# Kernel optimization log

Hardware: AMD Instinct MI355X
Metric: run time of the kernel (lower is better)

The kernel has to match this reference:

```python
import jax, jax.numpy as jnp
import numpy as np

B, T, D = 16384, 3, 512   # batch, task_num, input_dim
G = T + 1                  # expert groups (idx 0 shared)
NE = 4                     # experts per group
H, E = 512, 256            # expert hidden, expert output dim (layers=[512,256])
GH = 256                   # gate hidden
TH, TO = 128, 64           # tower hidden / output dims


def setup_inputs() -> dict:
    key = jax.random.key(0)
    ks = jax.random.split(key, 14)
    s = 0.02
    return {
        "inputs": jax.random.normal(ks[0], (B, G, D), jnp.float32),
        # expert MLPs: [group, expert, ...]
        "expert_W1": jax.random.normal(ks[1], (G, NE, D, H), jnp.float32) * s,
        "expert_b1": jnp.zeros((G, NE, H), jnp.float32),
        "expert_W2": jax.random.normal(ks[2], (G, NE, H, E), jnp.float32) * s,
        "expert_b2": jnp.zeros((G, NE, E), jnp.float32),
        # per-task gates (softmax over G*NE experts)
        "gate_W1": jax.random.normal(ks[3], (T, D, GH), jnp.float32) * s,
        "gate_b1": jnp.zeros((T, GH), jnp.float32),
        "gate_W2": jax.random.normal(ks[4], (T, GH, G * NE), jnp.float32) * s,
        "gate_b2": jnp.zeros((T, G * NE), jnp.float32),
        # per-task towers (is_last=True)
        "tower_W1": jax.random.normal(ks[5], (T, E, TH), jnp.float32) * s,
        "tower_b1": jnp.zeros((T, TH), jnp.float32),
        "tower_W2": jax.random.normal(ks[6], (T, TH, TO), jnp.float32) * s,
        "tower_b2": jnp.zeros((T, TO), jnp.float32),
    }


def reference(inputs, expert_W1, expert_b1, expert_W2, expert_b2,
              gate_W1, gate_b1, gate_W2, gate_b2,
              tower_W1, tower_b1, tower_W2, tower_b2):
    b = inputs.shape[0]
    g, ne = expert_W1.shape[0], expert_W1.shape[1]
    t_num = gate_W1.shape[0]

    # All expert groups in one batched einsum: [B, G, NE, E]
    h1 = jax.nn.relu(jnp.einsum('bgd,gndh->bgnh', inputs, expert_W1) + expert_b1)
    emb = jnp.einsum('bgnh,gnhe->bgne', h1, expert_W2) + expert_b2

    # Task gates on (task input + shared input): softmax over G*NE experts
    gin = inputs[:, 1:, :] + inputs[:, :1, :]                      # [B, T, D]
    gh = jax.nn.relu(jnp.einsum('btd,tdh->bth', gin, gate_W1) + gate_b1)
    gw = jax.nn.softmax(jnp.einsum('bth,thk->btk', gh, gate_W2) + gate_b2, axis=-1)  # [B,T,G*NE]

    emb_sg = jax.lax.stop_gradient(emb)
    group_ids = jnp.arange(g)
    outs = []
    for t in range(t_num):
        # gradient flows only through shared group (0) and own group (t+1)
        keep = (group_ids == 0) | (group_ids == t + 1)              # [G]
        masked = jnp.where(keep[None, :, None, None], emb, emb_sg)  # [B,G,NE,E]
        agg = jnp.einsum('bk,bke->be', gw[:, t], masked.reshape(b, g * ne, -1))  # [B,E]
        th = jax.nn.relu(agg @ tower_W1[t] + tower_b1[t])
        outs.append(th @ tower_W2[t] + tower_b2[t])                 # [B,TO]
    return jnp.concatenate(outs, axis=1)                           # [B, T*TO]
```

## Files before the change

### kernel.cpp

```cpp
#include <hip/hip_runtime.h>
#include <math.h>

#define B_N  16384
#define T_N  3
#define D_N  512
#define G_N  4
#define NE_N 4
#define H_N  512
#define E_N  256
#define GH_N 256
#define K16  16
#define TH_N 128
#define TO_N 64

typedef __attribute__((ext_vector_type(8))) short short8;
typedef __attribute__((ext_vector_type(4))) float floatx4;

__device__ __forceinline__ unsigned short f2bf(float f) {
    union { float f; unsigned u; } v; v.f = f;
    unsigned r = (v.u + 0x7fffu + ((v.u >> 16) & 1u)) >> 16;
    return (unsigned short)r;
}
__device__ __forceinline__ float bf2f(unsigned short h) {
    union { unsigned u; float f; } v; v.u = ((unsigned)h) << 16;
    return v.f;
}
__device__ __forceinline__ unsigned pack2(float lo, float hi) {
    return ((unsigned)f2bf(hi) << 16) | (unsigned)f2bf(lo);
}

typedef const __attribute__((address_space(1))) void gvoid_t;
typedef __attribute__((address_space(3))) void lvoid_t;

#if __has_builtin(__builtin_amdgcn_global_load_lds)
#define HAVE_GLL 1
__device__ __forceinline__ void load_lds16(const void* g, void* l) {
    __builtin_amdgcn_global_load_lds((gvoid_t*)g, (lvoid_t*)l, 16, 0, 0);
}
#else
#define HAVE_GLL 0
#endif

__global__ __launch_bounds__(256) void convert_inputs(
    const float* __restrict__ x, unsigned short* __restrict__ xb,
    unsigned short* __restrict__ ginb)
{
    const long b = blockIdx.x;
    const int tid = threadIdx.x;
    const float* xr = x + b * (G_N * D_N);
    unsigned short* xo = xb + b * (G_N * D_N);
    unsigned short* go = ginb + b * (T_N * D_N);
    float2 v0 = *(const float2*)&xr[tid * 2];
    *(unsigned*)&xo[tid * 2] = pack2(v0.x, v0.y);
    #pragma unroll
    for (int g = 1; g < G_N; ++g) {
        float2 v = *(const float2*)&xr[g * D_N + tid * 2];
        *(unsigned*)&xo[g * D_N + tid * 2] = pack2(v.x, v.y);
        *(unsigned*)&go[(g - 1) * D_N + tid * 2] = pack2(v.x + v0.x, v.y + v0.y);
    }
}

__global__ __launch_bounds__(256) void transpose_w(
    const float* __restrict__ in, unsigned short* __restrict__ out, int K, int N)
{
    __shared__ float tile[32][33];
    const int tx = threadIdx.x, ty = threadIdx.y;
    const long zo = (long)blockIdx.z * K * N;
    const int n0 = blockIdx.x * 32, k0 = blockIdx.y * 32;
    #pragma unroll
    for (int i = 0; i < 4; ++i)
        tile[ty + 8 * i][tx] = in[zo + (long)(k0 + ty + 8 * i) * N + n0 + tx];
    __syncthreads();
    #pragma unroll
    for (int i = 0; i < 4; ++i)
        out[zo + (long)(n0 + ty + 8 * i) * K + k0 + tx] = f2bf(tile[tx][ty + 8 * i]);
}

template<int RELU>
__global__ __launch_bounds__(256) void gemm_bf16(
    const unsigned short* __restrict__ A, int lda, int a_zoff,
    const unsigned short* __restrict__ Bt, int bt_zoff,
    const float* __restrict__ bias, int bias_zoff,
    unsigned short* __restrict__ C, int ldc, int c_zoff, int K)
{
    __shared__ __align__(16) unsigned short As[2][128 * 32];
    __shared__ __align__(16) unsigned short Bs[2][128 * 32];
    const int tid = threadIdx.x;
    const int z = blockIdx.z;
    const long m0 = (long)blockIdx.x * 128;
    const long n0 = (long)blockIdx.y * 128;
    const unsigned short* Ab = A + (long)z * a_zoff + m0 * lda;
    const unsigned short* Bb = Bt + (long)z * bt_zoff + n0 * K;
    const int lane16 = tid & 15;
    const int quad = (tid & 63) >> 4;
    const int wave = tid >> 6;
    const int wm = (wave >> 1) * 64;
    const int wn = (wave & 1) * 64;
    const int srow = tid >> 2;
    const int scolsw = (((tid & 3) ^ ((tid >> 3) & 3)) * 8);
    const int cw8 = ((quad ^ ((lane16 >> 1) & 3)) * 8);

    floatx4 acc[4][4] = {};

    for (int k0 = 0; k0 < K; k0 += 64) {
        #pragma unroll
        for (int h = 0; h < 2; ++h) {
            const int kh = k0 + h * 32;
#if HAVE_GLL
            load_lds16(Ab + (long)srow * lda + kh + scolsw, &As[h][tid * 8]);
            load_lds16(Ab + (long)(srow + 64) * lda + kh + scolsw, &As[h][2048 + tid * 8]);
            load_lds16(Bb + (long)srow * K + kh + scolsw, &Bs[h][tid * 8]);
            load_lds16(Bb + (long)(srow + 64) * K + kh + scolsw, &Bs[h][2048 + tid * 8]);
#else
            *(uint4*)&As[h][tid * 8] = *(const uint4*)(Ab + (long)srow * lda + kh + scolsw);
            *(uint4*)&As[h][2048 + tid * 8] = *(const uint4*)(Ab + (long)(srow + 64) * lda + kh + scolsw);
            *(uint4*)&Bs[h][tid * 8] = *(const uint4*)(Bb + (long)srow * K + kh + scolsw);
            *(uint4*)&Bs[h][2048 + tid * 8] = *(const uint4*)(Bb + (long)(srow + 64) * K + kh + scolsw);
#endif
        }
        __syncthreads();
        #pragma unroll
        for (int h = 0; h < 2; ++h) {
            short8 a[4], b[4];
            #pragma unroll
            for (int mi = 0; mi < 4; ++mi)
                a[mi] = *(const short8*)&As[h][(wm + mi * 16 + lane16) * 32 + cw8];
            #pragma unroll
            for (int ni = 0; ni < 4; ++ni)
                b[ni] = *(const short8*)&Bs[h][(wn + ni * 16 + lane16) * 32 + cw8];
            #pragma unroll
            for (int mi = 0; mi < 4; ++mi)
                #pragma unroll
                for (int ni = 0; ni < 4; ++ni)
                    acc[mi][ni] = __builtin_amdgcn_mfma_f32_16x16x32_bf16(
                        a[mi], b[ni], acc[mi][ni], 0, 0, 0);
        }
        __syncthreads();
    }

    unsigned short* Cb = C + (long)z * c_zoff + m0 * ldc + n0;
    const float* bb = bias + (long)z * bias_zoff + n0;
    #pragma unroll
    for (int mi = 0; mi < 4; ++mi) {
        #pragma unroll
        for (int ni = 0; ni < 4; ++ni) {
            const int col = wn + ni * 16 + lane16;
            const float bv = bb[col];
            #pragma unroll
            for (int r = 0; r < 4; ++r) {
                const int row = wm + mi * 16 + quad * 4 + r;
                float v = acc[mi][ni][r] + bv;
                if (RELU) v = fmaxf(v, 0.0f);
                Cb[(long)row * ldc + col] = f2bf(v);
            }
        }
    }
}

__global__ __launch_bounds__(256, 2) void expert_fused(
    const unsigned short* __restrict__ xb,
    const unsigned short* __restrict__ W1t,
    const float* __restrict__ eb1,
    const unsigned short* __restrict__ W2t,
    const float* __restrict__ eb2,
    unsigned short* __restrict__ embb)
{
    __shared__ __align__(16) unsigned short sm[33792];
    unsigned short* As  = sm;
    unsigned short* Bs  = sm + 8192;
    unsigned short* h1s = sm + 16384;

    const int tid = threadIdx.x;
    const unsigned bid = blockIdx.x;
    const int e = ((bid & 7) << 1) | ((bid >> 3) & 1);
    const long m0 = (long)(bid >> 4) * 128;
    const int g = e >> 2;

    const unsigned short* Ab  = xb + m0 * 2048 + g * 512;
    const unsigned short* W1b = W1t + (long)e * (512 * 512);
    const unsigned short* W2b = W2t + (long)e * (256 * 512);

    const int lane16 = tid & 15;
    const int quad = (tid & 63) >> 4;
    const int wave = tid >> 6;
    const int wm  = (wave >> 1) * 64;
    const int wn  = (wave & 1) * 64;
    const int wn2 = (wave & 1) * 128;
    const int srow = tid >> 2;
    const int scolsw = (((tid & 3) ^ ((tid >> 3) & 3)) * 8);
    const int cw8 = ((quad ^ ((lane16 >> 1) & 3)) * 8);

    floatx4 acc2[4][8] = {};

    for (int nc = 0; nc < 4; ++nc) {
        const unsigned short* Bb = W1b + ((long)nc << 16);
        floatx4 acc[4][4] = {};
        for (int k0 = 0; k0 < 512; k0 += 64) {
            #pragma unroll
            for (int h = 0; h < 2; ++h) {
                const int kh = k0 + h * 32;
#if HAVE_GLL
                load_lds16(Ab + (long)srow * 2048 + kh + scolsw, &As[h * 4096 + tid * 8]);
                load_lds16(Ab + (long)(srow + 64) * 2048 + kh + scolsw, &As[h * 4096 + 2048 + tid * 8]);
                load_lds16(Bb + (long)srow * 512 + kh + scolsw, &Bs[h * 4096 + tid * 8]);
                load_lds16(Bb + (long)(srow + 64) * 512 + kh + scolsw, &Bs[h * 4096 + 2048 + tid * 8]);
#else
                *(uint4*)&As[h * 4096 + tid * 8] = *(const uint4*)(Ab + (long)srow * 2048 + kh + scolsw);
                *(uint4*)&As[h * 4096 + 2048 + tid * 8] = *(const uint4*)(Ab + (long)(srow + 64) * 2048 + kh + scolsw);
                *(uint4*)&Bs[h * 4096 + tid * 8] = *(const uint4*)(Bb + (long)srow * 512 + kh + scolsw);
                *(uint4*)&Bs[h * 4096 + 2048 + tid * 8] = *(const uint4*)(Bb + (long)(srow + 64) * 512 + kh + scolsw);
#endif
            }
            __syncthreads();
            #pragma unroll
            for (int h = 0; h < 2; ++h) {
                short8 b[4];
                #pragma unroll
                for (int ni = 0; ni < 4; ++ni)
                    b[ni] = *(const short8*)&Bs[h * 4096 + (wn + ni * 16 + lane16) * 32 + cw8];
                #pragma unroll
                for (int mi = 0; mi < 4; ++mi) {
                    short8 a = *(const short8*)&As[h * 4096 + (wm + mi * 16 + lane16) * 32 + cw8];
                    #pragma unroll
                    for (int ni = 0; ni < 4; ++ni)
                        acc[mi][ni] = __builtin_amdgcn_mfma_f32_16x16x32_bf16(
                            a, b[ni], acc[mi][ni], 0, 0, 0);
                }
            }
            __syncthreads();
        }
        #pragma unroll
        for (int mi = 0; mi < 4; ++mi) {
            #pragma unroll
            for (int ni = 0; ni < 4; ++ni) {
                const int col = wn + ni * 16 + lane16;
                const float bv = eb1[e * 512 + nc * 128 + col];
                #pragma unroll
                for (int r = 0; r < 4; ++r) {
                    const int row = wm + mi * 16 + quad * 4 + r;
                    h1s[row * 136 + col] = f2bf(fmaxf(acc[mi][ni][r] + bv, 0.0f));
                }
            }
        }
        __syncthreads();
        #pragma unroll
        for (int ks = 0; ks < 128; ks += 32) {
            #pragma unroll
            for (int i = 0; i < 4; ++i) {
#if HAVE_GLL
                load_lds16(W2b + (long)(srow + 64 * i) * 512 + nc * 128 + ks + scolsw,
                           &As[i * 2048 + tid * 8]);
#else
                *(uint4*)&As[i * 2048 + tid * 8] =
                    *(const uint4*)(W2b + (long)(srow + 64 * i) * 512 + nc * 128 + ks + scolsw);
#endif
            }
            __syncthreads();
            #pragma unroll
            for (int nh = 0; nh < 2; ++nh) {
                short8 b2[4];
                #pragma unroll
                for (int nj = 0; nj < 4; ++nj)
                    b2[nj] = *(const short8*)&As[(wn2 + nh * 64 + nj * 16 + lane16) * 32 + cw8];
                #pragma unroll
                for (int mi = 0; mi < 4; ++mi) {
                    short8 a2 = *(const short8*)&h1s[(wm + mi * 16 + lane16) * 136 + ks + quad * 8];
                    #pragma unroll
                    for (int nj = 0; nj < 4; ++nj)
                        acc2[mi][nh * 4 + nj] = __builtin_amdgcn_mfma_f32_16x16x32_bf16(
                            a2, b2[nj], acc2[mi][nh * 4 + nj], 0, 0, 0);
                }
            }
            __syncthreads();
        }
    }

    unsigned short* Cb = embb + m0 * 4096 + (long)e * 256;
    #pragma unroll
    for (int mi = 0; mi < 4; ++mi) {
        #pragma unroll
        for (int j = 0; j < 8; ++j) {
            const int col = wn2 + (j >> 2) * 64 + (j & 3) * 16 + lane16;
            const float bv = eb2[e * 256 + col];
            #pragma unroll
            for (int r = 0; r < 4; ++r) {
                const int row = wm + mi * 16 + quad * 4 + r;
                Cb[(long)row * 4096 + col] = f2bf(acc2[mi][j][r] + bv);
            }
        }
    }
}

__global__ __launch_bounds__(256) void gate2_softmax(
    const unsigned short* __restrict__ gh, const float* __restrict__ W2,
    const float* __restrict__ b2, float* __restrict__ gw)
{
    const int t = blockIdx.y;
    const long b0 = (long)blockIdx.x * 64;
    const int tid = threadIdx.x;
    __shared__ __align__(16) unsigned short ghs[64 * 256];
    __shared__ float ls[64 * 16];
    #pragma unroll
    for (int it = 0; it < 8; ++it) {
        int seg = it * 256 + tid;
        int row = seg >> 5;
        int col = (seg & 31) * 8;
        *(uint4*)&ghs[seg * 8] =
            *(const uint4*)&gh[(b0 + row) * (T_N * GH_N) + (long)t * GH_N + col];
    }
    __syncthreads();
    const float* W2t = W2 + (long)t * GH_N * K16;
    #pragma unroll
    for (int it = 0; it < 4; ++it) {
        int o = it * 256 + tid;
        int b = o >> 4, k = o & 15;
        float acc = b2[t * K16 + k];
        #pragma unroll 8
        for (int h = 0; h < GH_N; ++h)
            acc += bf2f(ghs[b * 256 + h]) * W2t[h * K16 + k];
        ls[o] = acc;
    }
    __syncthreads();
    if (tid < 64) {
        float m = -1e30f;
        #pragma unroll
        for (int k = 0; k < 16; ++k) m = fmaxf(m, ls[tid * 16 + k]);
        float e[16], s = 0.f;
        #pragma unroll
        for (int k = 0; k < 16; ++k) { e[k] = expf(ls[tid * 16 + k] - m); s += e[k]; }
        const float inv = 1.0f / s;
        float* gwp = gw + (b0 + tid) * (T_N * K16) + (long)t * K16;
        #pragma unroll
        for (int k = 0; k < 16; ++k) gwp[k] = e[k] * inv;
    }
}

__global__ __launch_bounds__(256) void agg_kernel(
    const unsigned short* __restrict__ emb, const float* __restrict__ gw,
    unsigned short* __restrict__ aggb, long bc)
{
    const long b = (long)blockIdx.x * 8 + (threadIdx.x >> 5);
    const int e0 = (threadIdx.x & 31) * 8;
    const unsigned short* er = emb + b * 4096 + e0;
    const float* gwr = gw + b * 48;
    float a0[8] = {}, a1[8] = {}, a2[8] = {};
    #pragma unroll
    for (int k = 0; k < 16; ++k) {
        short8 v = *(const short8*)(er + (long)k * 256);
        const float w0 = gwr[k], w1 = gwr[16 + k], w2 = gwr[32 + k];
        #pragma unroll
        for (int j = 0; j < 8; ++j) {
            float f = bf2f((unsigned short)v[j]);
            a0[j] += w0 * f; a1[j] += w1 * f; a2[j] += w2 * f;
        }
    }
    unsigned r0[4] = {pack2(a0[0], a0[1]), pack2(a0[2], a0[3]),
                      pack2(a0[4], a0[5]), pack2(a0[6], a0[7])};
    unsigned r1[4] = {pack2(a1[0], a1[1]), pack2(a1[2], a1[3]),
                      pack2(a1[4], a1[5]), pack2(a1[6], a1[7])};
    unsigned r2[4] = {pack2(a2[0], a2[1]), pack2(a2[2], a2[3]),
                      pack2(a2[4], a2[5]), pack2(a2[6], a2[7])};
    *(uint4*)(aggb + 0L * bc * 256 + b * 256 + e0) = *(uint4*)r0;
    *(uint4*)(aggb + 1L * bc * 256 + b * 256 + e0) = *(uint4*)r1;
    *(uint4*)(aggb + 2L * bc * 256 + b * 256 + e0) = *(uint4*)r2;
}

__global__ __launch_bounds__(256) void tower_fused(
    const unsigned short* __restrict__ aggb, long bc,
    const unsigned short* __restrict__ w1t, const float* __restrict__ tb1,
    const unsigned short* __restrict__ w2t, const float* __restrict__ tb2,
    float* __restrict__ out)
{
    __shared__ __align__(16) unsigned short sm[26112];
    unsigned short* As  = sm;
    unsigned short* Bs  = sm + 4096;
    unsigned short* th  = sm;
    unsigned short* w2s = sm + 17408;
    const int tid = threadIdx.x;
    const int t = blockIdx.y;
    const long m0 = (long)blockIdx.x * 128;
    const unsigned short* Ab = aggb + (long)t * bc * 256 + m0 * 256;
    const unsigned short* Bb = w1t + (long)t * (TH_N * E_N);
    const int lane16 = tid & 15;
    const int quad = (tid & 63) >> 4;
    const int wave = tid >> 6;
    const int wm = (wave >> 1) * 64;
    const int wn = (wave & 1) * 64;
    const int srow = tid >> 2;
    const int scolsw = (((tid & 3) ^ ((tid >> 3) & 3)) * 8);
    const int cw8 = ((quad ^ ((lane16 >> 1) & 3)) * 8);

    #pragma unroll
    for (int i = 0; i < 4; ++i) {
        const int seg = i * 256 + tid;
        const int row = seg >> 4, cb = (seg & 15) * 8;
        *(uint4*)&w2s[row * 136 + cb] =
            *(const uint4*)&w2t[(long)t * (TO_N * TH_N) + (long)row * 128 + cb];
    }

    floatx4 acc[4][4] = {};
    for (int k0 = 0; k0 < 256; k0 += 32) {
#if HAVE_GLL
        load_lds16(Ab + (long)srow * 256 + k0 + scolsw, &As[tid * 8]);
        load_lds16(Ab + (long)(srow + 64) * 256 + k0 + scolsw, &As[2048 + tid * 8]);
        load_lds16(Bb + (long)srow * 256 + k0 + scolsw, &Bs[tid * 8]);
        load_lds16(Bb + (long)(srow + 64) * 256 + k0 + scolsw, &Bs[2048 + tid * 8]);
#else
        *(uint4*)&As[tid * 8] = *(const uint4*)(Ab + (long)srow * 256 + k0 + scolsw);
        *(uint4*)&As[2048 + tid * 8] = *(const uint4*)(Ab + (long)(srow + 64) * 256 + k0 + scolsw);
        *(uint4*)&Bs[tid * 8] = *(const uint4*)(Bb + (long)srow * 256 + k0 + scolsw);
        *(uint4*)&Bs[2048 + tid * 8] = *(const uint4*)(Bb + (long)(srow + 64) * 256 + k0 + scolsw);
#endif
        __syncthreads();
        short8 a[4], b[4];
        #pragma unroll
        for (int mi = 0; mi < 4; ++mi)
            a[mi] = *(const short8*)&As[(wm + mi * 16 + lane16) * 32 + cw8];
        #pragma unroll
        for (int ni = 0; ni < 4; ++ni)
            b[ni] = *(const short8*)&Bs[(wn + ni * 16 + lane16) * 32 + cw8];
        #pragma unroll
        for (int mi = 0; mi < 4; ++mi)
            #pragma unroll
            for (int ni = 0; ni < 4; ++ni)
                acc[mi][ni] = __builtin_amdgcn_mfma_f32_16x16x32_bf16(
                    a[mi], b[ni], acc[mi][ni], 0, 0, 0);
        __syncthreads();
    }

    #pragma unroll
    for (int mi = 0; mi < 4; ++mi) {
        #pragma unroll
        for (int ni = 0; ni < 4; ++ni) {
            const int col = wn + ni * 16 + lane16;
            const float bv = tb1[t * TH_N + col];
            #pragma unroll
            for (int r = 0; r < 4; ++r) {
                const int row = wm + mi * 16 + quad * 4 + r;
                th[row * 136 + col] = f2bf(fmaxf(acc[mi][ni][r] + bv, 0.0f));
            }
        }
    }
    __syncthreads();

    floatx4 acc2[2][4] = {};
    #pragma unroll
    for (int kk = 0; kk < 4; ++kk) {
        short8 a2[2], b2[4];
        #pragma unroll
        for (int mi = 0; mi < 2; ++mi)
            a2[mi] = *(const short8*)&th[(wave * 32 + mi * 16 + lane16) * 136 + kk * 32 + quad * 8];
        #pragma unroll
        for (int ni = 0; ni < 4; ++ni)
            b2[ni] = *(const short8*)&w2s[(ni * 16 + lane16) * 136 + kk * 32 + quad * 8];
        #pragma unroll
        for (int mi = 0; mi < 2; ++mi)
            #pragma unroll
            for (int ni = 0; ni < 4; ++ni)
                acc2[mi][ni] = __builtin_amdgcn_mfma_f32_16x16x32_bf16(
                    a2[mi], b2[ni], acc2[mi][ni], 0, 0, 0);
    }
    #pragma unroll
    for (int mi = 0; mi < 2; ++mi) {
        #pragma unroll
        for (int ni = 0; ni < 4; ++ni) {
            const int col = ni * 16 + lane16;
            const float bv = tb2[t * TO_N + col];
            #pragma unroll
            for (int r = 0; r < 4; ++r) {
                const int row = wave * 32 + mi * 16 + quad * 4 + r;
                out[(m0 + row) * (T_N * TO_N) + t * TO_N + col] = acc2[mi][ni][r] + bv;
            }
        }
    }
}

extern "C" void kernel_launch(void* const* d_in, const int* in_sizes, int n_in,
                              void* d_out, int out_size, void* d_ws, size_t ws_size,
                              hipStream_t stream)
{
    const float* x   = (const float*)d_in[0];
    const float* eW1 = (const float*)d_in[1];
    const float* eb1 = (const float*)d_in[2];
    const float* eW2 = (const float*)d_in[3];
    const float* eb2 = (const float*)d_in[4];
    const float* gW1 = (const float*)d_in[5];
    const float* gb1 = (const float*)d_in[6];
    const float* gW2 = (const float*)d_in[7];
    const float* gb2 = (const float*)d_in[8];
    const float* tW1 = (const float*)d_in[9];
    const float* tb1 = (const float*)d_in[10];
    const float* tW2 = (const float*)d_in[11];
    const float* tb2 = (const float*)d_in[12];
    float* out = (float*)d_out;

    char* ws = (char*)d_ws;
    unsigned short* W1t  = (unsigned short*)(ws + 0);
    unsigned short* W2t  = (unsigned short*)(ws + 8388608);
    unsigned short* G1t  = (unsigned short*)(ws + 12582912);
    unsigned short* TW1t = (unsigned short*)(ws + 13369344);
    unsigned short* TW2t = (unsigned short*)(ws + 13565952);
    const size_t WFIX = 13615104;

    long BCo = 0;
    for (long co = 16384; co >= 128; co >>= 1)
        if (WFIX + (size_t)co * 18624 <= ws_size) { BCo = co; break; }
    if (BCo == 0) return;

    char* p = ws + WFIX;
    unsigned short* xb   = (unsigned short*)p; p += BCo * 4096;
    unsigned short* ginb = (unsigned short*)p; p += BCo * 3072;
    unsigned short* embb = (unsigned short*)p; p += BCo * 8192;
    unsigned short* gh   = (unsigned short*)p; p += BCo * 1536;
    float*          gw   = (float*)p;          p += BCo * 192;
    unsigned short* aggb = (unsigned short*)p;

    transpose_w<<<dim3(16, 16, 16), dim3(32, 8), 0, stream>>>(eW1, W1t, 512, 512);
    transpose_w<<<dim3(8, 16, 16), dim3(32, 8), 0, stream>>>(eW2, W2t, 512, 256);
    transpose_w<<<dim3(8, 16, 3), dim3(32, 8), 0, stream>>>(gW1, G1t, 512, 256);
    transpose_w<<<dim3(4, 8, 3), dim3(32, 8), 0, stream>>>(tW1, TW1t, 256, 128);
    transpose_w<<<dim3(2, 4, 3), dim3(32, 8), 0, stream>>>(tW2, TW2t, 128, 64);

    const long n_o = B_N / BCo;
    for (long c = 0; c < n_o; ++c) {
        const float* xc = x + c * BCo * (G_N * D_N);
        float* outc = out + c * BCo * (T_N * TO_N);

        convert_inputs<<<BCo, 256, 0, stream>>>(xc, xb, ginb);
        gemm_bf16<1><<<dim3(BCo / 128, 2, 3), 256, 0, stream>>>(
            ginb, 1536, 512, G1t, 131072, gb1, 256, gh, 768, 256, 512);
        gate2_softmax<<<dim3(BCo / 64, 3), 256, 0, stream>>>(gh, gW2, gb2, gw);
        expert_fused<<<dim3((BCo / 128) * 16), 256, 0, stream>>>(
            xb, W1t, eb1, W2t, eb2, embb);
        agg_kernel<<<BCo / 8, 256, 0, stream>>>(embb, gw, aggb, BCo);
        tower_fused<<<dim3(BCo / 128, 3), 256, 0, stream>>>(
            aggb, BCo, TW1t, tb1, TW2t, tb2, outc);
    }
}
```

Baseline: 608.2 us.

## Process two experts per block sharing a 64-row input tile

The fused expert kernel now has each block handle a 64-row batch panel for a pair of experts from the same group. The two wave-halves each compute one expert while sharing the staged input tile in LDS. Previously a block handled 128 rows for a single expert. The aim is to reuse the input tile across the two experts in a group and reduce redundant global input loads. In exchange, per-block weight traffic doubles relative to rows processed, LDS use grows, and the grid size changes.

```diff
diff --git a/kernel.cpp b/kernel.cpp
--- a/kernel.cpp
+++ b/kernel.cpp
@@ -165,67 +165,85 @@
     const float* __restrict__ eb2,
     unsigned short* __restrict__ embb)
 {
-    __shared__ __align__(16) unsigned short sm[33792];
+    __shared__ __align__(16) unsigned short sm[37376];
     unsigned short* As  = sm;
-    unsigned short* Bs  = sm + 8192;
-    unsigned short* h1s = sm + 16384;
+    unsigned short* Ws  = sm + 4096;
+    unsigned short* W2s = sm;
+    unsigned short* h1s = sm + 20480;
 
     const int tid = threadIdx.x;
     const unsigned bid = blockIdx.x;
-    const int e = ((bid & 7) << 1) | ((bid >> 3) & 1);
-    const long m0 = (long)(bid >> 4) * 128;
-    const int g = e >> 2;
-
-    const unsigned short* Ab  = xb + m0 * 2048 + g * 512;
-    const unsigned short* W1b = W1t + (long)e * (512 * 512);
-    const unsigned short* W2b = W2t + (long)e * (256 * 512);
+    const int pair = bid & 7;
+    const long panel = bid >> 3;
+    const int e0 = pair << 1;
+    const int g = pair >> 1;
+
+    const unsigned short* Ab  = xb + panel * 64 * 2048 + g * 512;
+    const unsigned short* W1b = W1t + (long)e0 * (512 * 512);
+    const unsigned short* W2b = W2t + (long)e0 * (256 * 512);
 
     const int lane16 = tid & 15;
     const int quad = (tid & 63) >> 4;
     const int wave = tid >> 6;
-    const int wm  = (wave >> 1) * 64;
+    const int half = wave >> 1;
+    const int e = e0 + half;
     const int wn  = (wave & 1) * 64;
     const int wn2 = (wave & 1) * 128;
     const int srow = tid >> 2;
-    const int scolsw = (((tid & 3) ^ ((tid >> 3) & 3)) * 8);
+    const int scol = (((tid & 3) ^ ((tid >> 3) & 3)) * 8);
     const int cw8 = ((quad ^ ((lane16 >> 1) & 3)) * 8);
+    unsigned short* h1e = h1s + half * 8448;
 
     floatx4 acc2[4][8] = {};
 
     for (int nc = 0; nc < 4; ++nc) {
-        const unsigned short* Bb = W1b + ((long)nc << 16);
         floatx4 acc[4][4] = {};
         for (int k0 = 0; k0 < 512; k0 += 64) {
             #pragma unroll
             for (int h = 0; h < 2; ++h) {
-                const int kh = k0 + h * 32;
 #if HAVE_GLL
-                load_lds16(Ab + (long)srow * 2048 + kh + scolsw, &As[h * 4096 + tid * 8]);
-                load_lds16(Ab + (long)(srow + 64) * 2048 + kh + scolsw, &As[h * 4096 + 2048 + tid * 8]);
-                load_lds16(Bb + (long)srow * 512 + kh + scolsw, &Bs[h * 4096 + tid * 8]);
-                load_lds16(Bb + (long)(srow + 64) * 512 + kh + scolsw, &Bs[h * 4096 + 2048 + tid * 8]);
+                load_lds16(Ab + (long)srow * 2048 + k0 + h * 32 + scol,
+                           &As[h * 2048 + tid * 8]);
 #else
-                *(uint4*)&As[h * 4096 + tid * 8] = *(const uint4*)(Ab + (long)srow * 2048 + kh + scolsw);
-                *(uint4*)&As[h * 4096 + 2048 + tid * 8] = *(const uint4*)(Ab + (long)(srow + 64) * 2048 + kh + scolsw);
-                *(uint4*)&Bs[h * 4096 + tid * 8] = *(const uint4*)(Bb + (long)srow * 512 + kh + scolsw);
-                *(uint4*)&Bs[h * 4096 + 2048 + tid * 8] = *(const uint4*)(Bb + (long)(srow + 64) * 512 + kh + scolsw);
+                *(uint4*)&As[h * 2048 + tid * 8] =
+                    *(const uint4*)(Ab + (long)srow * 2048 + k0 + h * 32 + scol);
 #endif
             }
+            #pragma unroll
+            for (int ee = 0; ee < 2; ++ee) {
+                const unsigned short* Wb = W1b + (long)ee * (512 * 512)
+                                         + (long)(nc * 128) * 512;
+                #pragma unroll
+                for (int h = 0; h < 2; ++h) {
+                    #pragma unroll
+                    for (int s = 0; s < 2; ++s) {
+#if HAVE_GLL
+                        load_lds16(Wb + (long)(srow + 64 * s) * 512 + k0 + h * 32 + scol,
+                                   &Ws[ee * 8192 + h * 4096 + (s * 256 + tid) * 8]);
+#else
+                        *(uint4*)&Ws[ee * 8192 + h * 4096 + (s * 256 + tid) * 8] =
+                            *(const uint4*)(Wb + (long)(srow + 64 * s) * 512 + k0 + h * 32 + scol);
+#endif
+                    }
+                }
+            }
             __syncthreads();
             #pragma unroll
             for (int h = 0; h < 2; ++h) {
-                short8 b[4];
+                short8 a[4], b[4];
+                #pragma unroll
+                for (int mi = 0; mi < 4; ++mi)
+                    a[mi] = *(const short8*)&As[h * 2048 + (mi * 16 + lane16) * 32 + cw8];
                 #pragma unroll
                 for (int ni = 0; ni < 4; ++ni)
-                    b[ni] = *(const short8*)&Bs[h * 4096 + (wn + ni * 16 + lane16) * 32 + cw8];
-                #pragma unroll
-                for (int mi = 0; mi < 4; ++mi) {
-                    short8 a = *(const short8*)&As[h * 4096 + (wm + mi * 16 + lane16) * 32 + cw8];
+                    b[ni] = *(const short8*)&Ws[half * 8192 + h * 4096
+                                                + (wn + ni * 16 + lane16) * 32 + cw8];
+                #pragma unroll
+                for (int mi = 0; mi < 4; ++mi)
                     #pragma unroll
                     for (int ni = 0; ni < 4; ++ni)
                         acc[mi][ni] = __builtin_amdgcn_mfma_f32_16x16x32_bf16(
-                            a, b[ni], acc[mi][ni], 0, 0, 0);
-                }
+                            a[mi], b[ni], acc[mi][ni], 0, 0, 0);
             }
             __syncthreads();
         }
@@ -237,8 +255,8 @@
                 const float bv = eb1[e * 512 + nc * 128 + col];
                 #pragma unroll
                 for (int r = 0; r < 4; ++r) {
-                    const int row = wm + mi * 16 + quad * 4 + r;
-                    h1s[row * 136 + col] = f2bf(fmaxf(acc[mi][ni][r] + bv, 0.0f));
+                    const int row = mi * 16 + quad * 4 + r;
+                    h1e[row * 132 + col] = f2bf(fmaxf(acc[mi][ni][r] + bv, 0.0f));
                 }
             }
         }
@@ -246,36 +264,43 @@
         #pragma unroll
         for (int ks = 0; ks < 128; ks += 32) {
             #pragma unroll
-            for (int i = 0; i < 4; ++i) {
+            for (int ee = 0; ee < 2; ++ee) {
+                const unsigned short* Wb = W2b + (long)ee * (256 * 512) + nc * 128 + ks;
+                #pragma unroll
+                for (int i = 0; i < 4; ++i) {
 #if HAVE_GLL
-                load_lds16(W2b + (long)(srow + 64 * i) * 512 + nc * 128 + ks + scolsw,
-                           &As[i * 2048 + tid * 8]);
+                    load_lds16(Wb + (long)(srow + 64 * i) * 512 + scol,
+                               &W2s[ee * 8192 + (i * 256 + tid) * 8]);
 #else
-                *(uint4*)&As[i * 2048 + tid * 8] =
-                    *(const uint4*)(W2b + (long)(srow + 64 * i) * 512 + nc * 128 + ks + scolsw);
+                    *(uint4*)&W2s[ee * 8192 + (i * 256 + tid) * 8] =
+                        *(const uint4*)(Wb + (long)(srow + 64 * i) * 512 + scol);
 #endif
+                }
             }
             __syncthreads();
+            short8 a2[4];
+            #pragma unroll
+            for (int mi = 0; mi < 4; ++mi)
+                a2[mi] = *(const short8*)&h1e[(mi * 16 + lane16) * 132 + ks + quad * 8];
             #pragma unroll
             for (int nh = 0; nh < 2; ++nh) {
                 short8 b2[4];
                 #pragma unroll
                 for (int nj = 0; nj < 4; ++nj)
-                    b2[nj] = *(const short8*)&As[(wn2 + nh * 64 + nj * 16 + lane16) * 32 + cw8];
-                #pragma unroll
-                for (int mi = 0; mi < 4; ++mi) {
-                    short8 a2 = *(const short8*)&h1s[(wm + mi * 16 + lane16) * 136 + ks + quad * 8];
+                    b2[nj] = *(const short8*)&W2s[half * 8192
+                        + (wn2 + nh * 64 + nj * 16 + lane16) * 32 + cw8];
+                #pragma unroll
+                for (int mi = 0; mi < 4; ++mi)
                     #pragma unroll
                     for (int nj = 0; nj < 4; ++nj)
                         acc2[mi][nh * 4 + nj] = __builtin_amdgcn_mfma_f32_16x16x32_bf16(
-                            a2, b2[nj], acc2[mi][nh * 4 + nj], 0, 0, 0);
-                }
+                            a2[mi], b2[nj], acc2[mi][nh * 4 + nj], 0, 0, 0);
             }
             __syncthreads();
         }
     }
 
-    unsigned short* Cb = embb + m0 * 4096 + (long)e * 256;
+    unsigned short* Cb = embb + panel * 64 * 4096 + (long)e * 256;
     #pragma unroll
     for (int mi = 0; mi < 4; ++mi) {
         #pragma unroll
@@ -284,7 +309,7 @@
             const float bv = eb2[e * 256 + col];
             #pragma unroll
             for (int r = 0; r < 4; ++r) {
-                const int row = wm + mi * 16 + quad * 4 + r;
+                const int row = mi * 16 + quad * 4 + r;
                 Cb[(long)row * 4096 + col] = f2bf(acc2[mi][j][r] + bv);
             }
         }
@@ -530,7 +555,7 @@
         gemm_bf16<1><<<dim3(BCo / 128, 2, 3), 256, 0, stream>>>(
             ginb, 1536, 512, G1t, 131072, gb1, 256, gh, 768, 256, 512);
         gate2_softmax<<<dim3(BCo / 64, 3), 256, 0, stream>>>(gh, gW2, gb2, gw);
-        expert_fused<<<dim3((BCo / 128) * 16), 256, 0, stream>>>(
+        expert_fused<<<dim3((BCo / 64) * 8), 256, 0, stream>>>(
             xb, W1t, eb1, W2t, eb2, embb);
         agg_kernel<<<BCo / 8, 256, 0, stream>>>(embb, gw, aggb, BCo);
         tower_fused<<<dim3(BCo / 128, 3), 256, 0, stream>>>(
```

Measured after the change: 665.9 us. 9.5% more time.
